# Performance work log

Hardware: AMD Instinct MI355X
Metric: run time of the kernel (lower is better)

Reference implementation:

```python
import jax, jax.numpy as jnp
import numpy as np
from itertools import product

GRID = 256          # voxels per axis
SCALE = 0.005       # regular grid spacing (transform diagonal)
OFFSET = -0.64      # grid origin (transform translation)
K = 2_000_000       # number of query points


def setup_inputs() -> dict:
    key = jax.random.key(0)
    kx, kv = jax.random.split(key)
    # query points uniform in [-0.6, 0.6]^3 (inside grid domain)
    x = (jax.random.uniform(kx, (K, 3), dtype=jnp.float32) - 0.5) * 1.2
    # SDF voxel grid values
    values = jax.random.normal(kv, (GRID, GRID, GRID), dtype=jnp.float32)
    # regular per-axis grid point coordinates (as in get_grid_pts)
    ax = (jnp.arange(GRID, dtype=jnp.float32) * SCALE + OFFSET)
    return {"x": x, "values": values, "px": ax, "py": ax, "pz": ax}


def _trilinear_interp(pts_xyz, values, axes):
    # pts_xyz: [K,3]; values: [Nx,Ny,Nz]; axes: (px,py,pz) sorted 1D coords
    idxs, dists, overalls = [], [], []
    for d, p in enumerate(axes):
        c = pts_xyz[:, d]                               # [K]
        n = p.shape[0]
        # torch.bucketize(x, p) with right=False == searchsorted side='left'
        ir = jnp.searchsorted(p, c, side="left")
        ir = jnp.minimum(ir, n - 1)
        il = jnp.clip(ir - 1, 0, n - 1)
        dl = jnp.maximum(c - p[il], 0.0)
        dr = jnp.maximum(p[ir] - c, 0.0)
        both_zero = (dl == 0.0) & (dr == 0.0)           # exactly on a grid point
        dl = jnp.where(both_zero, 1.0, dl)
        dr = jnp.where(both_zero, 1.0, dr)
        idxs.append((il, ir))
        dists.append((dl, dr))
        overalls.append(dl + dr)
    numerator = 0.0
    for onoff in product([0, 1], repeat=3):             # 8 corners
        ix, iy, iz = (idx[o] for o, idx in zip(onoff, idxs))
        w = dists[0][1 - onoff[0]] * dists[1][1 - onoff[1]] * dists[2][1 - onoff[2]]
        numerator = numerator + values[ix, iy, iz] * w
    denominator = overalls[0] * overalls[1] * overalls[2]
    return numerator / denominator                      # [K]


def reference(x, values, px, py, pz):
    pts = x.reshape(-1, 3).astype(jnp.float32)
    return _trilinear_interp(pts, values, (px, py, pz))  # squeezed [K]
```

## Files before the change

### kernel.cpp

```cpp
#include <hip/hip_runtime.h>

#define GRIDN 256
#define BPA 8
#define NBINS (BPA * BPA * BPA)
#define CAP 6144
#define HALF 2
#define CAPH (CAP / HALF)
#define CURSOR_STRIDE 16
#define FKEYS 512


__device__ __forceinline__ int cell_guess(float c) {
    float t = (c + 0.64f) * 200.0f;
    int i = (int)t;
    return min(max(i, 0), GRIDN - 1);
}

__device__ __forceinline__ void dim_interp(float c, const float* __restrict__ p,
                                           int& il, int& ir, float& dl, float& dr) {
    const float SCALE = 0.005f;
    const float OFFSET = -0.64f;
    float t = (c - OFFSET) * (1.0f / SCALE);
    int i = (int)ceilf(t);
    i = min(max(i, 0), GRIDN - 1);
    while (i < GRIDN - 1 && p[i] < c) ++i;
    while (i > 0 && p[i - 1] >= c) --i;
    ir = i;
    il = max(i - 1, 0);
    dl = fmaxf(c - p[il], 0.0f);
    dr = fmaxf(p[ir] - c, 0.0f);
    if (dl == 0.0f && dr == 0.0f) { dl = 1.0f; dr = 1.0f; }
}

__device__ __forceinline__ void dim_interp_fast(float c, const float* __restrict__ pax,
                                                int& il, int& ir, float& dl, float& dr) {
    float t = (c + 0.64f) * 200.0f;
    int i0 = (int)ceilf(t);
    i0 = min(max(i0, 2), 254);
    float pm2 = pax[i0 - 2];
    float pm1 = pax[i0 - 1];
    float p00 = pax[i0];
    float pp1 = pax[i0 + 1];
    bool a = (pm1 >= c);
    bool b = (p00 >= c);
    ir = a ? (i0 - 1) : (b ? i0 : (i0 + 1));
    float pr = a ? pm1 : (b ? p00 : pp1);
    float pl = a ? pm2 : (b ? pm1 : p00);
    il = ir - 1;
    dl = fmaxf(c - pl, 0.0f);
    dr = fmaxf(pr - c, 0.0f);
}

__device__ __forceinline__ float interp_point_ax(float cx, float cy, float cz,
                                                 const float* __restrict__ values,
                                                 const float* __restrict__ ax,
                                                 const float* __restrict__ ay,
                                                 const float* __restrict__ az) {
    int ixl, ixr, iyl, iyr, izl, izr;
    float dxl, dxr, dyl, dyr, dzl, dzr;
    dim_interp(cx, ax, ixl, ixr, dxl, dxr);
    dim_interp(cy, ay, iyl, iyr, dyl, dyr);
    dim_interp(cz, az, izl, izr, dzl, dzr);
    int bxl = ixl << 16, bxr = ixr << 16;
    int byl = iyl << 8,  byr = iyr << 8;
    float num =
        values[bxl + byl + izl] * (dxr * dyr * dzr) +
        values[bxl + byl + izr] * (dxr * dyr * dzl) +
        values[bxl + byr + izl] * (dxr * dyl * dzr) +
        values[bxl + byr + izr] * (dxr * dyl * dzl) +
        values[bxr + byl + izl] * (dxl * dyr * dzr) +
        values[bxr + byl + izr] * (dxl * dyr * dzl) +
        values[bxr + byr + izl] * (dxl * dyl * dzr) +
        values[bxr + byr + izr] * (dxl * dyl * dzl);
    float den = (dxl + dxr) * (dyl + dyr) * (dzl + dzr);
    return num / den;
}

__device__ __forceinline__ float interp_zpair_fast(float cx, float cy, float cz,
                                                   const float* __restrict__ values,
                                                   const float* __restrict__ sax) {
    int ixl, ixr, iyl, iyr, izl, izr;
    float dxl, dxr, dyl, dyr, dzl, dzr;
    dim_interp_fast(cx, sax,             ixl, ixr, dxl, dxr);
    dim_interp_fast(cy, sax + GRIDN,     iyl, iyr, dyl, dyr);
    dim_interp_fast(cz, sax + 2 * GRIDN, izl, izr, dzl, dzr);

    int bxl = ixl << 16, bxr = ixr << 16;
    int byl = iyl << 8,  byr = iyr << 8;

    float2 vll, vlr, vrl, vrr;
    __builtin_memcpy(&vll, &values[bxl + byl + izl], 8);
    __builtin_memcpy(&vlr, &values[bxl + byr + izl], 8);
    __builtin_memcpy(&vrl, &values[bxr + byl + izl], 8);
    __builtin_memcpy(&vrr, &values[bxr + byr + izl], 8);

    float num =
        (dxr * dyr) * (vll.x * dzr + vll.y * dzl) +
        (dxr * dyl) * (vlr.x * dzr + vlr.y * dzl) +
        (dxl * dyr) * (vrl.x * dzr + vrl.y * dzl) +
        (dxl * dyl) * (vrr.x * dzr + vrr.y * dzl);
    float den = (dxl + dxr) * (dyl + dyr) * (dzl + dzr);
    return num / den;
}


__global__ __launch_bounds__(1024) void bin_scatter2(
        const float* __restrict__ x, int K,
        unsigned* __restrict__ cursor,
        float4* __restrict__ records,
        int* __restrict__ inv,
        const float* __restrict__ values,
        const float* __restrict__ px,
        const float* __restrict__ py,
        const float* __restrict__ pz,
        float* __restrict__ out) {
    __shared__ unsigned cnt[NBINS];
    __shared__ unsigned slotcur[NBINS];

    int base = blockIdx.x * 4096;
    int end = min(base + 4096, K);

    for (int t = threadIdx.x; t < NBINS; t += 1024) cnt[t] = 0;
    __syncthreads();

    for (int i = base + threadIdx.x; i < end; i += 1024) {
        int bx = cell_guess(x[3 * i]) >> 5;
        int by = cell_guess(x[3 * i + 1]) >> 5;
        int bz = cell_guess(x[3 * i + 2]) >> 5;
        atomicAdd(&cnt[(bx * BPA + by) * BPA + bz], 1u);
    }
    __syncthreads();

    for (int t = threadIdx.x; t < NBINS; t += 1024)
        slotcur[t] = cnt[t] ? ((unsigned)t * CAP +
                               atomicAdd(&cursor[t * CURSOR_STRIDE], cnt[t]))
                            : 0u;
    __syncthreads();

    for (int i = base + threadIdx.x; i < end; i += 1024) {
        float cx = x[3 * i], cy = x[3 * i + 1], cz = x[3 * i + 2];
        int bx = cell_guess(cx) >> 5;
        int by = cell_guess(cy) >> 5;
        int bz = cell_guess(cz) >> 5;
        int b = (bx * BPA + by) * BPA + bz;
        unsigned s = atomicAdd(&slotcur[b], 1u);
        if (s < (unsigned)((b + 1) * CAP)) {
            records[s] = make_float4(cx, cy, cz, 0.0f);
            inv[i] = (int)s;
        } else {
            inv[i] = -1;
            out[i] = interp_point_ax(cx, cy, cz, values, px, py, pz);
        }
    }
}


#define K2_THREADS 1024

__global__ __launch_bounds__(K2_THREADS) void interp_halfsort(
        const float4* __restrict__ records,
        const unsigned* __restrict__ cursor,
        const float* __restrict__ values,
        const float* __restrict__ px,
        const float* __restrict__ py,
        const float* __restrict__ pz,
        float* __restrict__ res) {
    __shared__ float sax[3 * GRIDN];
    __shared__ unsigned hist[FKEYS];
    __shared__ unsigned wsum[8];
    __shared__ unsigned short skeys[CAPH];
    __shared__ unsigned short order[CAPH];
    __shared__ float4 spt[CAPH];
    __shared__ float sres[CAPH];

    int nb = gridDim.x;
    int b = blockIdx.x;
    int q = nb >> 3;
    int lin = (b & 7) * q + (b >> 3);
    int bin = lin >> 1;
    int half = lin & 1;

    for (int t = threadIdx.x; t < GRIDN; t += K2_THREADS) {
        sax[t] = px[t];
        sax[GRIDN + t] = py[t];
        sax[2 * GRIDN + t] = pz[t];
    }
    for (int t = threadIdx.x; t < FKEYS; t += K2_THREADS) hist[t] = 0;
    __syncthreads();

    unsigned binstart = (unsigned)bin * CAP;
    int npts = min((int)cursor[bin * CURSOR_STRIDE], CAP);
    if (npts <= 0) return;

    int cnt_h = (npts + HALF - 1) / HALF;
    int lo = half * cnt_h;
    int n = min(npts, lo + cnt_h) - lo;
    if (n <= 0) return;
    unsigned base = binstart + lo;

    int cbx = (bin >> 6) << 5;
    int cby = ((bin >> 3) & 7) << 5;
    int cbz = (bin & 7) << 5;

    for (int pt = threadIdx.x; pt < n; pt += K2_THREADS) {
        float4 rec = records[base + pt];
        spt[pt] = rec;
        int fx = (cell_guess(rec.x) - cbx) >> 2;
        int fy = (cell_guess(rec.y) - cby) >> 2;
        int fz = (cell_guess(rec.z) - cbz) >> 2;
        fx = min(max(fx, 0), 7); fy = min(max(fy, 0), 7); fz = min(max(fz, 0), 7);
        int k = (((fx << 3) | fy) << 3) | fz;
        skeys[pt] = (unsigned short)k;
        atomicAdd(&hist[k], 1u);
    }
    __syncthreads();

    unsigned v = 0, s = 0;
    int lane = threadIdx.x & 63, w = threadIdx.x >> 6;
    if (threadIdx.x < FKEYS) {
        v = hist[threadIdx.x];
        s = v;
        for (int off = 1; off < 64; off <<= 1) {
            unsigned t = __shfl_up(s, off, 64);
            if (lane >= off) s += t;
        }
        if (lane == 63) wsum[w] = s;
    }
    __syncthreads();
    if (threadIdx.x == 0) {
        unsigned a = 0;
        for (int i = 0; i < 8; ++i) { unsigned t = wsum[i]; wsum[i] = a; a += t; }
    }
    __syncthreads();
    if (threadIdx.x < FKEYS) hist[threadIdx.x] = s - v + wsum[w];
    __syncthreads();

    for (int pt = threadIdx.x; pt < n; pt += K2_THREADS) {
        unsigned slot = atomicAdd(&hist[skeys[pt]], 1u);
        order[slot] = (unsigned short)pt;
    }
    __syncthreads();

    for (int pt = threadIdx.x; pt < n; pt += K2_THREADS) {
        int j = order[pt];
        float4 r = spt[j];
        sres[j] = interp_zpair_fast(r.x, r.y, r.z, values, sax);
    }
    __syncthreads();

    for (int pt = threadIdx.x; pt < n; pt += K2_THREADS)
        res[base + pt] = sres[pt];
}


__global__ void unscatter(const int* __restrict__ inv,
                          const float* __restrict__ res,
                          float* __restrict__ out, int K) {
    int i = blockIdx.x * blockDim.x + threadIdx.x;
    if (i >= K) return;
    int s = inv[i];
    if (s >= 0) out[i] = res[s];
}


__global__ void trilerp_direct(const float* __restrict__ x,
                               const float* __restrict__ values,
                               const float* __restrict__ px,
                               const float* __restrict__ py,
                               const float* __restrict__ pz,
                               float* __restrict__ out, int K) {
    int i = blockIdx.x * blockDim.x + threadIdx.x;
    if (i >= K) return;
    out[i] = interp_point_ax(x[3 * i], x[3 * i + 1], x[3 * i + 2],
                             values, px, py, pz);
}

extern "C" void kernel_launch(void* const* d_in, const int* in_sizes, int n_in,
                              void* d_out, int out_size, void* d_ws, size_t ws_size,
                              hipStream_t stream) {
    const float* x      = (const float*)d_in[0];
    const float* values = (const float*)d_in[1];
    const float* px     = (const float*)d_in[2];
    const float* py     = (const float*)d_in[3];
    const float* pz     = (const float*)d_in[4];
    float* out = (float*)d_out;

    int K = in_sizes[0] / 3;

    size_t cursor_bytes  = (size_t)NBINS * CURSOR_STRIDE * 4;
    size_t records_bytes = (size_t)NBINS * CAP * 16;
    size_t inv_bytes     = (size_t)K * 4;
    size_t res_bytes     = (size_t)NBINS * CAP * 4;
    size_t need = cursor_bytes + records_bytes + inv_bytes + res_bytes;

    if (ws_size < need) {
        int grid = (K + 255) / 256;
        trilerp_direct<<<grid, 256, 0, stream>>>(x, values, px, py, pz, out, K);
        return;
    }

    char* p = (char*)d_ws;
    unsigned* cursor = (unsigned*)p;  p += cursor_bytes;
    float4* records  = (float4*)p;    p += records_bytes;
    int* inv         = (int*)p;       p += inv_bytes;
    float* res       = (float*)p;

    hipMemsetAsync(cursor, 0, cursor_bytes, stream);

    int nblk1 = (K + 4095) / 4096;
    bin_scatter2<<<nblk1, 1024, 0, stream>>>(x, K, cursor, records, inv,
                                             values, px, py, pz, out);

    interp_halfsort<<<NBINS * HALF, K2_THREADS, 0, stream>>>(records, cursor,
                                                             values, px, py, pz, res);

    int nblk3 = (K + 255) / 256;
    unscatter<<<nblk3, 256, 0, stream>>>(inv, res, out, K);
}
```

Before: 84.88 us.

## Scatter sorted points directly into LDS and give each wave a contiguous chunk

The per-bin counting sort no longer keeps key and order arrays. Records are re-read from global memory in a second pass and written straight into their sorted LDS slot, with the original index packed into the w component. Interpolation then splits the sorted points into contiguous per-wave chunks and processes two points per lane per iteration, which improves locality of the voxel gathers within each wave and exposes more memory-level parallelism. The cost is a second global read of the records and a cell-key recomputation in exchange for less LDS traffic and fewer passes.

```diff
diff --git a/kernel.cpp b/kernel.cpp
--- a/kernel.cpp
+++ b/kernel.cpp
@@ -157,7 +157,7 @@
 
 #define K2_THREADS 1024
 
-__global__ __launch_bounds__(K2_THREADS) void interp_halfsort(
+__global__ __launch_bounds__(K2_THREADS) void interp_wavechunk(
         const float4* __restrict__ records,
         const unsigned* __restrict__ cursor,
         const float* __restrict__ values,
@@ -168,9 +168,7 @@
     __shared__ float sax[3 * GRIDN];
     __shared__ unsigned hist[FKEYS];
     __shared__ unsigned wsum[8];
-    __shared__ unsigned short skeys[CAPH];
-    __shared__ unsigned short order[CAPH];
-    __shared__ float4 spt[CAPH];
+    __shared__ float4 spts[CAPH];
     __shared__ float sres[CAPH];
 
     int nb = gridDim.x;
@@ -204,14 +202,11 @@
 
     for (int pt = threadIdx.x; pt < n; pt += K2_THREADS) {
         float4 rec = records[base + pt];
-        spt[pt] = rec;
         int fx = (cell_guess(rec.x) - cbx) >> 2;
         int fy = (cell_guess(rec.y) - cby) >> 2;
         int fz = (cell_guess(rec.z) - cbz) >> 2;
         fx = min(max(fx, 0), 7); fy = min(max(fy, 0), 7); fz = min(max(fz, 0), 7);
-        int k = (((fx << 3) | fy) << 3) | fz;
-        skeys[pt] = (unsigned short)k;
-        atomicAdd(&hist[k], 1u);
+        atomicAdd(&hist[(((fx << 3) | fy) << 3) | fz], 1u);
     }
     __syncthreads();
 
@@ -236,15 +231,31 @@
     __syncthreads();
 
     for (int pt = threadIdx.x; pt < n; pt += K2_THREADS) {
-        unsigned slot = atomicAdd(&hist[skeys[pt]], 1u);
-        order[slot] = (unsigned short)pt;
-    }
-    __syncthreads();
-
-    for (int pt = threadIdx.x; pt < n; pt += K2_THREADS) {
-        int j = order[pt];
-        float4 r = spt[j];
-        sres[j] = interp_zpair_fast(r.x, r.y, r.z, values, sax);
+        float4 rec = records[base + pt];
+        int fx = (cell_guess(rec.x) - cbx) >> 2;
+        int fy = (cell_guess(rec.y) - cby) >> 2;
+        int fz = (cell_guess(rec.z) - cbz) >> 2;
+        fx = min(max(fx, 0), 7); fy = min(max(fy, 0), 7); fz = min(max(fz, 0), 7);
+        unsigned slot = atomicAdd(&hist[(((fx << 3) | fy) << 3) | fz], 1u);
+        spts[slot] = make_float4(rec.x, rec.y, rec.z, __int_as_float(pt));
+    }
+    __syncthreads();
+
+    {
+        int wid = threadIdx.x >> 6;
+        int chunk = (n + 15) >> 4;
+        int clo = wid * chunk;
+        int chi = min(n, clo + chunk);
+        for (int pt = clo + lane; pt < chi; pt += 128) {
+            float4 r0 = spts[pt];
+            int pt1 = pt + 64;
+            bool has1 = (pt1 < chi);
+            float4 r1 = has1 ? spts[pt1] : r0;
+            float v0 = interp_zpair_fast(r0.x, r0.y, r0.z, values, sax);
+            float v1 = interp_zpair_fast(r1.x, r1.y, r1.z, values, sax);
+            sres[__float_as_int(r0.w)] = v0;
+            if (has1) sres[__float_as_int(r1.w)] = v1;
+        }
     }
     __syncthreads();
 
@@ -311,8 +322,8 @@
     bin_scatter2<<<nblk1, 1024, 0, stream>>>(x, K, cursor, records, inv,
                                              values, px, py, pz, out);
 
-    interp_halfsort<<<NBINS * HALF, K2_THREADS, 0, stream>>>(records, cursor,
-                                                             values, px, py, pz, res);
+    interp_wavechunk<<<NBINS * HALF, K2_THREADS, 0, stream>>>(records, cursor,
+                                                              values, px, py, pz, res);
 
     int nblk3 = (K + 255) / 256;
     unscatter<<<nblk3, 256, 0, stream>>>(inv, res, out, K);
```

New measurement: 88.32 us. 4.0% more time.
